# Optimization experiments

Hardware: AMD Instinct MI355X
Metric: run time of the kernel (lower is better)

The kernel has to match this reference:

```python
import jax, jax.numpy as jnp
import numpy as np

N = 50000
E = 800000
IN_C, HID_C, OUT_C = 128, 96, 40
NEG_SLOPE = 0.2


def _glorot(key, shape):
    fan_in, fan_out = shape[0], shape[-1]
    lim = jnp.sqrt(6.0 / (fan_in + fan_out))
    return jax.random.uniform(key, shape, jnp.float32, -lim, lim)


def setup_inputs() -> dict:
    key = jax.random.key(0)
    ks = jax.random.split(key, 12)
    x = jax.random.normal(ks[0], (N, IN_C), jnp.float32)
    edge_index = jax.random.randint(ks[1], (2, E), 0, N, jnp.int64)
    new_edge_indexs = jax.random.randint(ks[2], (2, 1000), 0, N, jnp.int64)
    # GATConv layer 1 params (heads=1)
    W1 = _glorot(ks[3], (IN_C, HID_C))
    a_src1 = _glorot(ks[4], (HID_C,))
    a_dst1 = _glorot(ks[5], (HID_C,))
    b1 = jnp.zeros((HID_C,), jnp.float32)
    # GATConv layer 2 params
    W2 = _glorot(ks[6], (HID_C, OUT_C))
    a_src2 = _glorot(ks[7], (OUT_C,))
    a_dst2 = _glorot(ks[8], (OUT_C,))
    b2 = jnp.zeros((OUT_C,), jnp.float32)
    return {"x": x, "edge_index": edge_index, "new_edge_indexs": new_edge_indexs,
            "W1": W1, "a_src1": a_src1, "a_dst1": a_dst1, "b1": b1,
            "W2": W2, "a_src2": a_src2, "a_dst2": a_dst2, "b2": b2}


def gat_conv(x, src, dst, W, a_src, a_dst, b):
    # h: [N, C_out] projected features
    h = x @ W
    alpha_src = h @ a_src  # [N]
    alpha_dst = h @ a_dst  # [N]
    # per-edge raw attention (gather)
    e = jax.nn.leaky_relu(alpha_src[src] + alpha_dst[dst], NEG_SLOPE)  # [E']
    # segment softmax over destination neighborhoods
    m = jax.ops.segment_max(e, dst, num_segments=N)
    w = jnp.exp(e - m[dst])
    s = jax.ops.segment_sum(w, dst, num_segments=N)
    alpha = w / s[dst]  # [E'] (self-loops guarantee s > 0)
    # scatter-add aggregation of weighted source features
    out = jax.ops.segment_sum(h[src] * alpha[:, None], dst, num_segments=N)
    return out + b


def reference(x, edge_index, new_edge_indexs, W1, a_src1, a_dst1, b1,
              W2, a_src2, a_dst2, b2):
    # PyG GATConv default add_self_loops=True
    loops = jnp.arange(N, dtype=edge_index.dtype)
    src = jnp.concatenate([edge_index[0], loops])
    dst = jnp.concatenate([edge_index[1], loops])
    h = gat_conv(x, src, dst, W1, a_src1, a_dst1, b1)
    h = jax.nn.relu(h)
    # dropout p=0.5 is identity in eval mode
    h = gat_conv(h, src, dst, W2, a_src2, a_dst2, b2)
    return jax.nn.log_softmax(h, axis=-1)
```

## Files before the change

### kernel.cpp

```cpp
#include <hip/hip_runtime.h>
#include <math.h>

#define N_NODES 50000
#define N_EDGES 800000
#define N_ETOT  850000
#define C_IN    128
#define C_HID   96
#define C_OUT   40
#define NEG_SLOPE 0.2f
#define NSB ((N_NODES + 1023) / 1024)


__global__ void k_initdeg(int* __restrict__ deg) {
    int i = blockIdx.x * blockDim.x + threadIdx.x;
    if (i < N_NODES) deg[i] = 1;
}

__global__ void k_hist(const int* __restrict__ ei, int* __restrict__ deg) {
    int i = blockIdx.x * blockDim.x + threadIdx.x;
    if (i < N_EDGES) atomicAdd(&deg[ei[N_EDGES + i]], 1);
}

__global__ void k_scan1(const int* __restrict__ deg, int* __restrict__ rp,
                        int* __restrict__ bsum) {
    __shared__ int wsum[16];
    int t = threadIdx.x, lane = t & 63, w = t >> 6;
    int i = blockIdx.x * 1024 + t;
    int v = (i < N_NODES) ? deg[i] : 0;
    int inc = v;
    #pragma unroll
    for (int off = 1; off < 64; off <<= 1) {
        int u = __shfl_up(inc, off);
        if (lane >= off) inc += u;
    }
    if (lane == 63) wsum[w] = inc;
    __syncthreads();
    if (w == 0) {
        int sv = (lane < 16) ? wsum[lane] : 0;
        #pragma unroll
        for (int off = 1; off < 16; off <<= 1) {
            int u = __shfl_up(sv, off);
            if (lane >= off) sv += u;
        }
        if (lane < 16) wsum[lane] = sv;
    }
    __syncthreads();
    int exc = ((w == 0) ? 0 : wsum[w - 1]) + inc - v;
    if (i < N_NODES) rp[i] = exc;
    if (t == 0) bsum[blockIdx.x] = wsum[15];
}

__global__ void k_scan2(const int* __restrict__ bsum, int* __restrict__ boff,
                        int* __restrict__ rp) {
    int lane = threadIdx.x;
    int v = (lane < NSB) ? bsum[lane] : 0;
    int inc = v;
    #pragma unroll
    for (int off = 1; off < 64; off <<= 1) {
        int u = __shfl_up(inc, off);
        if (lane >= off) inc += u;
    }
    if (lane < NSB) boff[lane] = inc - v;
    if (lane == 63) rp[N_NODES] = inc;
}

__global__ void k_scan3(int* __restrict__ rp, const int* __restrict__ boff,
                        int* __restrict__ cursor) {
    int i = blockIdx.x * blockDim.x + threadIdx.x;
    if (i < N_NODES) {
        int v = rp[i] + boff[i >> 10];
        rp[i] = v; cursor[i] = v;
    }
}

__global__ void k_scatter(const int* __restrict__ ei, int* __restrict__ cursor,
                          int* __restrict__ csr_src) {
    int i = blockIdx.x * blockDim.x + threadIdx.x;
    if (i >= N_ETOT) return;
    int src, dst;
    if (i < N_EDGES) { src = ei[i]; dst = ei[N_EDGES + i]; }
    else             { src = dst = i - N_EDGES; }
    int pos = atomicAdd(&cursor[dst], 1);
    csr_src[pos] = src;
}


template<int CIN, int COUT, int KH, int CT, int NT, int NP>
__global__ __launch_bounds__(CT * NT)
void k_gemm(const float* __restrict__ X, const float* __restrict__ W,
            const float* __restrict__ asrc, const float* __restrict__ adst,
            float* __restrict__ H, float* __restrict__ as, float* __restrict__ ad) {
    constexpr int NPB = NT * NP;
    constexpr int BLK = CT * NT;
    constexpr int KQ  = CIN / 4;
    constexpr int CQ  = COUT / 4;
    __shared__ float xs[NPB][CIN + 1];
    __shared__ float4 Ws4[KH][CQ + 1];
    __shared__ float red[NPB * 2];
    const int t  = threadIdx.x;
    const int nb = blockIdx.x * NPB;

    for (int idx = t; idx < NPB * 2; idx += BLK) red[idx] = 0.f;

    for (int idx = t; idx < NPB * KQ; idx += BLK) {
        int n = idx / KQ, kq = idx - n * KQ;
        float4 v = make_float4(0.f, 0.f, 0.f, 0.f);
        if (nb + n < N_NODES)
            v = reinterpret_cast<const float4*>(X)[(size_t)(nb + n) * KQ + kq];
        xs[n][4 * kq + 0] = v.x; xs[n][4 * kq + 1] = v.y;
        xs[n][4 * kq + 2] = v.z; xs[n][4 * kq + 3] = v.w;
    }

    const int ct = t % CT, nt = t / CT;
    float acc[NP][4] = {};

    for (int kb = 0; kb < CIN; kb += KH) {
        __syncthreads();
        for (int idx = t; idx < KH * CQ; idx += BLK) {
            int kk = idx / CQ, c4 = idx - kk * CQ;
            Ws4[kk][c4] = reinterpret_cast<const float4*>(W)[(size_t)(kb + kk) * CQ + c4];
        }
        __syncthreads();
        #pragma unroll 4
        for (int kk = 0; kk < KH; ++kk) {
            float4 wv = Ws4[kk][ct];
            #pragma unroll
            for (int i = 0; i < NP; ++i) {
                float xv = xs[nt * NP + i][kb + kk];
                acc[i][0] = fmaf(xv, wv.x, acc[i][0]);
                acc[i][1] = fmaf(xv, wv.y, acc[i][1]);
                acc[i][2] = fmaf(xv, wv.z, acc[i][2]);
                acc[i][3] = fmaf(xv, wv.w, acc[i][3]);
            }
        }
    }

    float a0 = asrc[4*ct], a1 = asrc[4*ct+1], a2 = asrc[4*ct+2], a3 = asrc[4*ct+3];
    float d0 = adst[4*ct], d1 = adst[4*ct+1], d2 = adst[4*ct+2], d3 = adst[4*ct+3];
    #pragma unroll
    for (int i = 0; i < NP; ++i) {
        int n = nb + nt * NP + i;
        float pa = acc[i][0]*a0 + acc[i][1]*a1 + acc[i][2]*a2 + acc[i][3]*a3;
        float pd = acc[i][0]*d0 + acc[i][1]*d1 + acc[i][2]*d2 + acc[i][3]*d3;
        atomicAdd(&red[2 * (nt * NP + i)    ], pa);
        atomicAdd(&red[2 * (nt * NP + i) + 1], pd);
        if (n < N_NODES) {
            float4 o = make_float4(acc[i][0], acc[i][1], acc[i][2], acc[i][3]);
            reinterpret_cast<float4*>(H)[(size_t)n * CQ + ct] = o;
        }
    }
    __syncthreads();
    for (int idx = t; idx < NPB; idx += BLK) {
        int n = nb + idx;
        if (n < N_NODES) { as[n] = red[2 * idx]; ad[n] = red[2 * idx + 1]; }
    }
}


template<int C, int EPI>
__global__ __launch_bounds__(256)
void k_node_agg(const int* __restrict__ row_ptr, const int* __restrict__ csr_src,
                const float* __restrict__ as, const float* __restrict__ ad,
                const float* __restrict__ h, const float* __restrict__ bias,
                float* __restrict__ outp) {
    constexpr int CV    = C / 4;
    constexpr int SLOTS = 64 / CV;
    int n = blockIdx.x * 4 + (threadIdx.x >> 6);
    int lane = threadIdx.x & 63;
    int beg = row_ptr[n], end = row_ptr[n + 1];
    float adn = ad[n];

    float mx = -INFINITY;
    for (int j = beg + lane; j < end; j += 64) {
        float v = as[csr_src[j]] + adn;
        v = (v >= 0.f) ? v : NEG_SLOPE * v;
        mx = fmaxf(mx, v);
    }
    #pragma unroll
    for (int off = 32; off; off >>= 1) mx = fmaxf(mx, __shfl_xor(mx, off));

    const int slot = lane / CV;
    const int c    = lane - slot * CV;
    const float4* h4 = reinterpret_cast<const float4*>(h);

    float4 acc = make_float4(0.f, 0.f, 0.f, 0.f);
    float s_lane = 0.f;

    for (int j = beg; j < end; j += 2 * SLOTS) {
        int j0 = j + slot, j1 = j + SLOTS + slot;
        bool a0 = (slot < SLOTS) && (j0 < end);
        bool a1 = (slot < SLOTS) && (j1 < end);
        int s0 = a0 ? csr_src[j0] : 0;
        int s1 = a1 ? csr_src[j1] : 0;
        float4 g0 = make_float4(0.f,0.f,0.f,0.f), g1 = make_float4(0.f,0.f,0.f,0.f);
        if (a0) g0 = h4[(size_t)s0 * CV + c];
        if (a1) g1 = h4[(size_t)s1 * CV + c];
        float v0 = as[s0] + adn; v0 = (v0 >= 0.f) ? v0 : NEG_SLOPE * v0;
        float v1 = as[s1] + adn; v1 = (v1 >= 0.f) ? v1 : NEG_SLOPE * v1;
        float w0 = a0 ? __expf(v0 - mx) : 0.f;
        float w1 = a1 ? __expf(v1 - mx) : 0.f;
        if (c == 0) s_lane += w0 + w1;
        acc.x = fmaf(w0, g0.x, acc.x); acc.y = fmaf(w0, g0.y, acc.y);
        acc.z = fmaf(w0, g0.z, acc.z); acc.w = fmaf(w0, g0.w, acc.w);
        acc.x = fmaf(w1, g1.x, acc.x); acc.y = fmaf(w1, g1.y, acc.y);
        acc.z = fmaf(w1, g1.z, acc.z); acc.w = fmaf(w1, g1.w, acc.w);
    }

    float4 tot = acc;
    #pragma unroll
    for (int s = 1; s < SLOTS; ++s) {
        int sl = (lane + CV * s) & 63;
        tot.x += __shfl(acc.x, sl); tot.y += __shfl(acc.y, sl);
        tot.z += __shfl(acc.z, sl); tot.w += __shfl(acc.w, sl);
    }
    float s = s_lane;
    #pragma unroll
    for (int off = 32; off; off >>= 1) s += __shfl_xor(s, off);
    float inv = 1.f / s;

    const float4* b4 = reinterpret_cast<const float4*>(bias);
    if (EPI == 0) {
        if (lane < CV) {
            float4 bb = b4[lane];
            float4 o;
            o.x = fmaxf(fmaf(tot.x, inv, bb.x), 0.f);
            o.y = fmaxf(fmaf(tot.y, inv, bb.y), 0.f);
            o.z = fmaxf(fmaf(tot.z, inv, bb.z), 0.f);
            o.w = fmaxf(fmaf(tot.w, inv, bb.w), 0.f);
            reinterpret_cast<float4*>(outp)[(size_t)n * CV + lane] = o;
        }
    } else {
        bool actw = lane < CV;
        float4 v4 = make_float4(-INFINITY, -INFINITY, -INFINITY, -INFINITY);
        if (actw) {
            float4 bb = b4[lane];
            v4.x = fmaf(tot.x, inv, bb.x); v4.y = fmaf(tot.y, inv, bb.y);
            v4.z = fmaf(tot.z, inv, bb.z); v4.w = fmaf(tot.w, inv, bb.w);
        }
        float vm = fmaxf(fmaxf(v4.x, v4.y), fmaxf(v4.z, v4.w));
        #pragma unroll
        for (int off = 32; off; off >>= 1) vm = fmaxf(vm, __shfl_xor(vm, off));
        float es = actw ? (__expf(v4.x - vm) + __expf(v4.y - vm) +
                           __expf(v4.z - vm) + __expf(v4.w - vm)) : 0.f;
        #pragma unroll
        for (int off = 32; off; off >>= 1) es += __shfl_xor(es, off);
        float lse = vm + logf(es);
        if (actw) {
            float4 o = make_float4(v4.x - lse, v4.y - lse, v4.z - lse, v4.w - lse);
            reinterpret_cast<float4*>(outp)[(size_t)n * CV + lane] = o;
        }
    }
}


extern "C" void kernel_launch(void* const* d_in, const int* in_sizes, int n_in,
                              void* d_out, int out_size, void* d_ws, size_t ws_size,
                              hipStream_t stream) {
    const float* x      = (const float*)d_in[0];
    const int*   ei     = (const int*)d_in[1];
    const float* W1     = (const float*)d_in[3];
    const float* a_src1 = (const float*)d_in[4];
    const float* a_dst1 = (const float*)d_in[5];
    const float* b1     = (const float*)d_in[6];
    const float* W2     = (const float*)d_in[7];
    const float* a_src2 = (const float*)d_in[8];
    const float* a_dst2 = (const float*)d_in[9];
    const float* b2     = (const float*)d_in[10];
    float* out = (float*)d_out;

    float* wsf = (float*)d_ws;
    size_t off = 0;
    float* h1  = wsf + off; off += (size_t)N_NODES * C_HID;
    float* x2  = wsf + off; off += (size_t)N_NODES * C_HID;
    float* h2  = wsf + off; off += (size_t)N_NODES * C_OUT;
    float* as1 = wsf + off; off += N_NODES;
    float* ad1 = wsf + off; off += N_NODES;
    float* as2 = wsf + off; off += N_NODES;
    float* ad2 = wsf + off; off += N_NODES;
    int* wsi     = (int*)(wsf + off);
    size_t ioff  = 0;
    int* deg     = wsi + ioff; ioff += N_NODES;
    int* row_ptr = wsi + ioff; ioff += N_NODES + 1;
    int* cursor  = wsi + ioff; ioff += N_NODES;
    int* csr_src = wsi + ioff; ioff += N_ETOT;
    int* bsum    = wsi + ioff; ioff += NSB;
    int* boff    = wsi + ioff; ioff += NSB;

    k_initdeg<<<(N_NODES + 255) / 256, 256, 0, stream>>>(deg);
    k_hist<<<(N_EDGES + 255) / 256, 256, 0, stream>>>(ei, deg);
    k_scan1<<<NSB, 1024, 0, stream>>>(deg, row_ptr, bsum);
    k_scan2<<<1, 64, 0, stream>>>(bsum, boff, row_ptr);
    k_scan3<<<(N_NODES + 1023) / 1024, 1024, 0, stream>>>(row_ptr, boff, cursor);
    k_scatter<<<(N_ETOT + 255) / 256, 256, 0, stream>>>(ei, cursor, csr_src);

    k_gemm<C_IN, C_HID, 32, 24, 8, 4><<<(N_NODES + 31) / 32, 192, 0, stream>>>(
        x, W1, a_src1, a_dst1, h1, as1, ad1);
    k_node_agg<C_HID, 0><<<N_NODES / 4, 256, 0, stream>>>(row_ptr, csr_src, as1, ad1, h1, b1, x2);

    k_gemm<C_HID, C_OUT, 96, 10, 32, 2><<<(N_NODES + 63) / 64, 320, 0, stream>>>(
        x2, W2, a_src2, a_dst2, h2, as2, ad2);
    k_node_agg<C_OUT, 1><<<N_NODES / 4, 256, 0, stream>>>(row_ptr, csr_src, as2, ad2, h2, b2, out);
}
```

Measured before the change: 347.6 us.

## Store projected features in bf16 and reuse per-edge weights via wave shuffles

```diff
diff --git a/kernel.cpp b/kernel.cpp
--- a/kernel.cpp
+++ b/kernel.cpp
@@ -9,6 +9,14 @@
 #define C_OUT   40
 #define NEG_SLOPE 0.2f
 #define NSB ((N_NODES + 1023) / 1024)
+
+__device__ __forceinline__ unsigned short f2bf(float f) {
+    unsigned u = __float_as_uint(f);
+    u = u + 0x7fffu + ((u >> 16) & 1u);
+    return (unsigned short)(u >> 16);
+}
+__device__ __forceinline__ float bfu_lo(unsigned g) { return __uint_as_float(g << 16); }
+__device__ __forceinline__ float bfu_hi(unsigned g) { return __uint_as_float(g & 0xffff0000u); }
 
 
 __global__ void k_initdeg(int* __restrict__ deg) {
@@ -89,7 +97,7 @@
 __global__ __launch_bounds__(CT * NT)
 void k_gemm(const float* __restrict__ X, const float* __restrict__ W,
             const float* __restrict__ asrc, const float* __restrict__ adst,
-            float* __restrict__ H, float* __restrict__ as, float* __restrict__ ad) {
+            unsigned short* __restrict__ Hb, float* __restrict__ as, float* __restrict__ ad) {
     constexpr int NPB = NT * NP;
     constexpr int BLK = CT * NT;
     constexpr int KQ  = CIN / 4;
@@ -145,8 +153,10 @@
         atomicAdd(&red[2 * (nt * NP + i)    ], pa);
         atomicAdd(&red[2 * (nt * NP + i) + 1], pd);
         if (n < N_NODES) {
-            float4 o = make_float4(acc[i][0], acc[i][1], acc[i][2], acc[i][3]);
-            reinterpret_cast<float4*>(H)[(size_t)n * CQ + ct] = o;
+            ushort4 o;
+            o.x = f2bf(acc[i][0]); o.y = f2bf(acc[i][1]);
+            o.z = f2bf(acc[i][2]); o.w = f2bf(acc[i][3]);
+            reinterpret_cast<ushort4*>(Hb)[(size_t)n * CQ + ct] = o;
         }
     }
     __syncthreads();
@@ -157,97 +167,132 @@
 }
 
 
-template<int C, int EPI>
+template<int C, int VEC, int UN, int EPI>
 __global__ __launch_bounds__(256)
-void k_node_agg(const int* __restrict__ row_ptr, const int* __restrict__ csr_src,
+void k_node_agg(const int* __restrict__ rp, const int* __restrict__ csr_src,
                 const float* __restrict__ as, const float* __restrict__ ad,
-                const float* __restrict__ h, const float* __restrict__ bias,
+                const void* __restrict__ hv, const float* __restrict__ bias,
                 float* __restrict__ outp) {
-    constexpr int CV    = C / 4;
-    constexpr int SLOTS = 64 / CV;
+    constexpr int CL    = C / VEC;
+    constexpr int SLOTS = 64 / CL;
     int n = blockIdx.x * 4 + (threadIdx.x >> 6);
     int lane = threadIdx.x & 63;
-    int beg = row_ptr[n], end = row_ptr[n + 1];
+    int beg = rp[n], end = rp[n + 1];
     float adn = ad[n];
 
-    float mx = -INFINITY;
-    for (int j = beg + lane; j < end; j += 64) {
-        float v = as[csr_src[j]] + adn;
-        v = (v >= 0.f) ? v : NEG_SLOPE * v;
-        mx = fmaxf(mx, v);
+    int j0 = beg + lane;
+    int sj = (j0 < end) ? csr_src[j0] : 0;
+    float v = as[sj] + adn; v = (v >= 0.f) ? v : NEG_SLOPE * v;
+    float mx = (j0 < end) ? v : -INFINITY;
+    for (int j = j0 + 64; j < end; j += 64) {
+        int s2 = csr_src[j];
+        float v2 = as[s2] + adn; v2 = (v2 >= 0.f) ? v2 : NEG_SLOPE * v2;
+        mx = fmaxf(mx, v2);
     }
     #pragma unroll
     for (int off = 32; off; off >>= 1) mx = fmaxf(mx, __shfl_xor(mx, off));
 
-    const int slot = lane / CV;
-    const int c    = lane - slot * CV;
-    const float4* h4 = reinterpret_cast<const float4*>(h);
-
-    float4 acc = make_float4(0.f, 0.f, 0.f, 0.f);
+    const int slot = lane / CL;
+    const int c    = lane - slot * CL;
+    const bool slotok = slot < SLOTS;
+
+    float acc[VEC];
+    #pragma unroll
+    for (int k = 0; k < VEC; ++k) acc[k] = 0.f;
     float s_lane = 0.f;
 
-    for (int j = beg; j < end; j += 2 * SLOTS) {
-        int j0 = j + slot, j1 = j + SLOTS + slot;
-        bool a0 = (slot < SLOTS) && (j0 < end);
-        bool a1 = (slot < SLOTS) && (j1 < end);
-        int s0 = a0 ? csr_src[j0] : 0;
-        int s1 = a1 ? csr_src[j1] : 0;
-        float4 g0 = make_float4(0.f,0.f,0.f,0.f), g1 = make_float4(0.f,0.f,0.f,0.f);
-        if (a0) g0 = h4[(size_t)s0 * CV + c];
-        if (a1) g1 = h4[(size_t)s1 * CV + c];
-        float v0 = as[s0] + adn; v0 = (v0 >= 0.f) ? v0 : NEG_SLOPE * v0;
-        float v1 = as[s1] + adn; v1 = (v1 >= 0.f) ? v1 : NEG_SLOPE * v1;
-        float w0 = a0 ? __expf(v0 - mx) : 0.f;
-        float w1 = a1 ? __expf(v1 - mx) : 0.f;
-        if (c == 0) s_lane += w0 + w1;
-        acc.x = fmaf(w0, g0.x, acc.x); acc.y = fmaf(w0, g0.y, acc.y);
-        acc.z = fmaf(w0, g0.z, acc.z); acc.w = fmaf(w0, g0.w, acc.w);
-        acc.x = fmaf(w1, g1.x, acc.x); acc.y = fmaf(w1, g1.y, acc.y);
-        acc.z = fmaf(w1, g1.z, acc.z); acc.w = fmaf(w1, g1.w, acc.w);
-    }
-
-    float4 tot = acc;
+    for (int cb = beg; cb < end; cb += 64) {
+        int cnt = min(64, end - cb);
+        float w;
+        if (cb == beg) {
+            w = (j0 < end) ? __expf(v - mx) : 0.f;
+        } else {
+            int j = cb + lane;
+            int s2 = (j < end) ? csr_src[j] : 0;
+            float v2 = as[s2] + adn; v2 = (v2 >= 0.f) ? v2 : NEG_SLOPE * v2;
+            w = (j < end) ? __expf(v2 - mx) : 0.f;
+            sj = s2;
+        }
+        s_lane += w;
+
+        for (int base = 0; base < cnt; base += SLOTS * UN) {
+            #pragma unroll
+            for (int u = 0; u < UN; ++u) {
+                int jj = base + u * SLOTS + slot;
+                bool act = slotok && (jj < cnt);
+                int jjc = act ? jj : 0;
+                int   srcu = __shfl(sj, jjc);
+                float wu   = __shfl(w,  jjc);
+                if (act) {
+                    if constexpr (VEC == 8) {
+                        int4 g = reinterpret_cast<const int4*>(hv)[(size_t)srcu * CL + c];
+                        acc[0] = fmaf(wu, bfu_lo(g.x), acc[0]);
+                        acc[1] = fmaf(wu, bfu_hi(g.x), acc[1]);
+                        acc[2] = fmaf(wu, bfu_lo(g.y), acc[2]);
+                        acc[3] = fmaf(wu, bfu_hi(g.y), acc[3]);
+                        acc[4] = fmaf(wu, bfu_lo(g.z), acc[4]);
+                        acc[5] = fmaf(wu, bfu_hi(g.z), acc[5]);
+                        acc[6] = fmaf(wu, bfu_lo(g.w), acc[6]);
+                        acc[7] = fmaf(wu, bfu_hi(g.w), acc[7]);
+                    } else {
+                        uint2 g = reinterpret_cast<const uint2*>(hv)[(size_t)srcu * CL + c];
+                        acc[0] = fmaf(wu, bfu_lo(g.x), acc[0]);
+                        acc[1] = fmaf(wu, bfu_hi(g.x), acc[1]);
+                        acc[2] = fmaf(wu, bfu_lo(g.y), acc[2]);
+                        acc[3] = fmaf(wu, bfu_hi(g.y), acc[3]);
+                    }
+                }
+            }
+        }
+    }
+
+    float tot[VEC];
+    #pragma unroll
+    for (int k = 0; k < VEC; ++k) tot[k] = acc[k];
     #pragma unroll
     for (int s = 1; s < SLOTS; ++s) {
-        int sl = (lane + CV * s) & 63;
-        tot.x += __shfl(acc.x, sl); tot.y += __shfl(acc.y, sl);
-        tot.z += __shfl(acc.z, sl); tot.w += __shfl(acc.w, sl);
-    }
-    float s = s_lane;
-    #pragma unroll
-    for (int off = 32; off; off >>= 1) s += __shfl_xor(s, off);
-    float inv = 1.f / s;
-
-    const float4* b4 = reinterpret_cast<const float4*>(bias);
+        int sl = (lane + CL * s) & 63;
+        #pragma unroll
+        for (int k = 0; k < VEC; ++k) tot[k] += __shfl(acc[k], sl);
+    }
+    float ssum = s_lane;
+    #pragma unroll
+    for (int off = 32; off; off >>= 1) ssum += __shfl_xor(ssum, off);
+    float inv = 1.f / ssum;
+
     if (EPI == 0) {
-        if (lane < CV) {
-            float4 bb = b4[lane];
-            float4 o;
-            o.x = fmaxf(fmaf(tot.x, inv, bb.x), 0.f);
-            o.y = fmaxf(fmaf(tot.y, inv, bb.y), 0.f);
-            o.z = fmaxf(fmaf(tot.z, inv, bb.z), 0.f);
-            o.w = fmaxf(fmaf(tot.w, inv, bb.w), 0.f);
-            reinterpret_cast<float4*>(outp)[(size_t)n * CV + lane] = o;
+        if (lane < CL) {
+            const float* b = bias + lane * VEC;
+            float4* o = reinterpret_cast<float4*>(outp) + (size_t)n * (C / 4) + lane * (VEC / 4);
+            #pragma unroll
+            for (int q = 0; q < VEC / 4; ++q) {
+                float4 ov;
+                ov.x = fmaxf(fmaf(tot[4*q+0], inv, b[4*q+0]), 0.f);
+                ov.y = fmaxf(fmaf(tot[4*q+1], inv, b[4*q+1]), 0.f);
+                ov.z = fmaxf(fmaf(tot[4*q+2], inv, b[4*q+2]), 0.f);
+                ov.w = fmaxf(fmaf(tot[4*q+3], inv, b[4*q+3]), 0.f);
+                o[q] = ov;
+            }
         }
     } else {
-        bool actw = lane < CV;
-        float4 v4 = make_float4(-INFINITY, -INFINITY, -INFINITY, -INFINITY);
+        bool actw = lane < CL;
+        float v0 = -INFINITY, v1 = -INFINITY, v2 = -INFINITY, v3 = -INFINITY;
         if (actw) {
-            float4 bb = b4[lane];
-            v4.x = fmaf(tot.x, inv, bb.x); v4.y = fmaf(tot.y, inv, bb.y);
-            v4.z = fmaf(tot.z, inv, bb.z); v4.w = fmaf(tot.w, inv, bb.w);
-        }
-        float vm = fmaxf(fmaxf(v4.x, v4.y), fmaxf(v4.z, v4.w));
+            const float* b = bias + lane * 4;
+            v0 = fmaf(tot[0], inv, b[0]); v1 = fmaf(tot[1], inv, b[1]);
+            v2 = fmaf(tot[2], inv, b[2]); v3 = fmaf(tot[3], inv, b[3]);
+        }
+        float vm = fmaxf(fmaxf(v0, v1), fmaxf(v2, v3));
         #pragma unroll
         for (int off = 32; off; off >>= 1) vm = fmaxf(vm, __shfl_xor(vm, off));
-        float es = actw ? (__expf(v4.x - vm) + __expf(v4.y - vm) +
-                           __expf(v4.z - vm) + __expf(v4.w - vm)) : 0.f;
+        float es = actw ? (__expf(v0 - vm) + __expf(v1 - vm) +
+                           __expf(v2 - vm) + __expf(v3 - vm)) : 0.f;
         #pragma unroll
         for (int off = 32; off; off >>= 1) es += __shfl_xor(es, off);
         float lse = vm + logf(es);
         if (actw) {
-            float4 o = make_float4(v4.x - lse, v4.y - lse, v4.z - lse, v4.w - lse);
-            reinterpret_cast<float4*>(outp)[(size_t)n * CV + lane] = o;
+            float4 ov = make_float4(v0 - lse, v1 - lse, v2 - lse, v3 - lse);
+            reinterpret_cast<float4*>(outp)[(size_t)n * (C / 4) + lane] = ov;
         }
     }
 }
@@ -270,13 +315,13 @@
 
     float* wsf = (float*)d_ws;
     size_t off = 0;
-    float* h1  = wsf + off; off += (size_t)N_NODES * C_HID;
     float* x2  = wsf + off; off += (size_t)N_NODES * C_HID;
-    float* h2  = wsf + off; off += (size_t)N_NODES * C_OUT;
     float* as1 = wsf + off; off += N_NODES;
     float* ad1 = wsf + off; off += N_NODES;
     float* as2 = wsf + off; off += N_NODES;
     float* ad2 = wsf + off; off += N_NODES;
+    unsigned short* h1 = (unsigned short*)(wsf + off); off += (size_t)N_NODES * C_HID / 2;
+    unsigned short* h2 = (unsigned short*)(wsf + off); off += (size_t)N_NODES * C_OUT / 2;
     int* wsi     = (int*)(wsf + off);
     size_t ioff  = 0;
     int* deg     = wsi + ioff; ioff += N_NODES;
@@ -295,9 +340,11 @@
 
     k_gemm<C_IN, C_HID, 32, 24, 8, 4><<<(N_NODES + 31) / 32, 192, 0, stream>>>(
         x, W1, a_src1, a_dst1, h1, as1, ad1);
-    k_node_agg<C_HID, 0><<<N_NODES / 4, 256, 0, stream>>>(row_ptr, csr_src, as1, ad1, h1, b1, x2);
+    k_node_agg<C_HID, 8, 2, 0><<<N_NODES / 4, 256, 0, stream>>>(
+        row_ptr, csr_src, as1, ad1, h1, b1, x2);
 
     k_gemm<C_HID, C_OUT, 96, 10, 32, 2><<<(N_NODES + 63) / 64, 320, 0, stream>>>(
         x2, W2, a_src2, a_dst2, h2, as2, ad2);
-    k_node_agg<C_OUT, 1><<<N_NODES / 4, 256, 0, stream>>>(row_ptr, csr_src, as2, ad2, h2, b2, out);
-}
+    k_node_agg<C_OUT, 4, 2, 1><<<N_NODES / 4, 256, 0, stream>>>(
+        row_ptr, csr_src, as2, ad2, h2, b2, out);
+}
```

After: 322.7 us. 1.08x faster.
